# Kernel tuning notes

Measured on AMD Instinct MI355X. Metric: run time of the kernel, lower is better.

Reference implementation:

```python
import jax, jax.numpy as jnp
import numpy as np

ALPHA = 0.001      # module init arg alpha
BETA = 1.0         # softness of k-means assignments
N_ITERS = 10       # fixed soft-kmeans iterations
EPS = 1e-8


def _pairwise_sq_dist(x, c):
    # x: [N, D], c: [K, D] -> [N, K] squared euclidean distances
    x2 = jnp.sum(x * x, axis=1, keepdims=True)          # [N, 1]
    c2 = jnp.sum(c * c, axis=1)[None, :]                # [1, K]
    d2 = x2 + c2 - 2.0 * (x @ c.T)
    return jnp.maximum(d2, 0.0)


def soft_kmeans(enc, K):
    # deterministic init: first K points as centroids
    C = enc[:K]
    r = None
    loss = jnp.array(0.0, dtype=enc.dtype)
    for _ in range(N_ITERS):
        d2 = _pairwise_sq_dist(enc, C)                  # [N, K]
        r = jax.nn.softmax(-BETA * d2, axis=1)          # soft assignments [N, K]
        loss = jnp.mean(jnp.sum(r * d2, axis=1))        # weighted within-cluster dist
        C = (r.T @ enc) / (jnp.sum(r, axis=0)[:, None] + EPS)  # centroid update [K, D]
    return C, r, loss


def setup_inputs() -> dict:
    key = jax.random.key(0)
    k1, k2, k3 = jax.random.split(key, 3)
    N, D_DATA, D_LAT = 65536, 512, 64
    X = jax.random.normal(k1, (N, D_DATA), dtype=jnp.float32)
    encoding = jax.random.normal(k2, (N, D_LAT), dtype=jnp.float32)
    decoding = jax.random.normal(k3, (N, D_DATA), dtype=jnp.float32)
    return {"X": X, "encoding": encoding, "decoding": decoding, "K": 64}


def reference(X, encoding, decoding, K):
    decoder_loss = jnp.mean((X - decoding) ** 2)        # F.mse_loss (mean reduction)
    _, _, cluster_loss = soft_kmeans(encoding, K)
    return decoder_loss + cluster_loss * ALPHA
```

## Files before the change

kernel.cpp:

```cpp
#include <hip/hip_runtime.h>

typedef __attribute__((ext_vector_type(8))) short bf16x8;
typedef __attribute__((ext_vector_type(4))) float f32x4;

#define NROWS   65536
#define NSLICE  8
#define SLICESZ 4160
#define SETSZ   (NSLICE*SLICESZ)
#define EPSV    1e-8f
#define RPITCH  264

#define WS_DEC   0
#define WS_LOSS  1
#define WS_SETS  16
#define WS_X2    (WS_SETS + 9*SETSZ)
#define WS_ENCB  (WS_X2 + NROWS)
#define WS_EBF   (WS_ENCB + 2097152)
#define WS_END   (WS_EBF + 2097152)

static __device__ __forceinline__ unsigned short f2bf(float f) {
    union { float f; unsigned u; } v; v.f = f;
    unsigned u = v.u + 0x7fffu + ((v.u >> 16) & 1u);
    return (unsigned short)(u >> 16);
}
static __device__ __forceinline__ float bf2f(unsigned short h) {
    union { unsigned u; float f; } v; v.u = ((unsigned)h) << 16; return v.f;
}
static __device__ __forceinline__ uint4 pack8(const unsigned short* h) {
    uint4 o;
    o.x = h[0] | ((unsigned)h[1] << 16);
    o.y = h[2] | ((unsigned)h[3] << 16);
    o.z = h[4] | ((unsigned)h[5] << 16);
    o.w = h[6] | ((unsigned)h[7] << 16);
    return o;
}

__global__ __launch_bounds__(256, 4) void decoder_loss_kernel(
    const float* __restrict__ X, const float* __restrict__ Dec,
    float* __restrict__ out_sum)
{
    const int stride = 8192 * 256;
    int i = blockIdx.x * 256 + threadIdx.x;
    const f32x4* X4 = (const f32x4*)X;
    const f32x4* D4 = (const f32x4*)Dec;
    f32x4 va[4], vb[4];
    #pragma unroll
    for (int u = 0; u < 4; ++u) va[u] = __builtin_nontemporal_load(&X4[i + u * stride]);
    #pragma unroll
    for (int u = 0; u < 4; ++u) vb[u] = __builtin_nontemporal_load(&D4[i + u * stride]);
    float s0 = 0.f, s1 = 0.f, s2 = 0.f, s3 = 0.f;
    #pragma unroll
    for (int u = 0; u < 4; ++u) {
        f32x4 d = va[u] - vb[u];
        s0 = fmaf(d.x, d.x, s0);
        s1 = fmaf(d.y, d.y, s1);
        s2 = fmaf(d.z, d.z, s2);
        s3 = fmaf(d.w, d.w, s3);
    }
    float s = (s0 + s1) + (s2 + s3);
    #pragma unroll
    for (int off = 32; off; off >>= 1) s += __shfl_down(s, off, 64);
    __shared__ float red[4];
    if ((threadIdx.x & 63) == 0) red[threadIdx.x >> 6] = s;
    __syncthreads();
    if (threadIdx.x == 0) atomicAdd(out_sum, red[0] + red[1] + red[2] + red[3]);
}

__global__ __launch_bounds__(256) void prep0(
    const float* __restrict__ enc, unsigned* __restrict__ encB,
    uint4* __restrict__ encBfrag, float* __restrict__ x2)
{
    __shared__ unsigned short L[64 * 64];
    int t = threadIdx.x;
    int rl = t >> 2, part = t & 3;
    int row = blockIdx.x * 64 + rl;
    const float4* src = (const float4*)(enc + (size_t)row * 64 + part * 16);
    unsigned short hv[16];
    float ss = 0.f;
    #pragma unroll
    for (int i = 0; i < 4; ++i) {
        float4 v = src[i];
        unsigned short a = f2bf(v.x), b = f2bf(v.y), c = f2bf(v.z), d = f2bf(v.w);
        hv[i*4+0] = a; hv[i*4+1] = b; hv[i*4+2] = c; hv[i*4+3] = d;
        float fa = bf2f(a), fb = bf2f(b), fc = bf2f(c), fd = bf2f(d);
        ss = fmaf(fa, fa, fmaf(fb, fb, fmaf(fc, fc, fmaf(fd, fd, ss))));
    }
    unsigned* dst = encB + ((size_t)row * 64 + part * 16) / 2;
    #pragma unroll
    for (int i = 0; i < 8; ++i) dst[i] = (unsigned)hv[2*i] | ((unsigned)hv[2*i+1] << 16);
    #pragma unroll
    for (int i = 0; i < 16; ++i) L[rl * 64 + part * 16 + i] = hv[i];
    ss += __shfl_xor(ss, 1, 64);
    ss += __shfl_xor(ss, 2, 64);
    if (part == 0) x2[row] = ss;
    __syncthreads();
    for (int e = t; e < 512; e += 256) {
        int rbl = e >> 8, dt = (e >> 6) & 3, lane = e & 63;
        int q = lane >> 4, c = lane & 15;
        unsigned short hw[8];
        #pragma unroll
        for (int j = 0; j < 8; ++j)
            hw[j] = L[(rbl * 32 + q * 8 + j) * 64 + dt * 16 + c];
        encBfrag[(size_t)blockIdx.x * 512 + e] = pack8(hw);
    }
}

__global__ __launch_bounds__(256, 3) void kmeans_main(
    const bf16x8* __restrict__ encB8, const bf16x8* __restrict__ encBfrag8,
    const float* __restrict__ enc, const float* __restrict__ prev_set,
    float* __restrict__ cur_set, const float* __restrict__ x2,
    float* __restrict__ loss_sum, int mode)
{
    __shared__ union {
        unsigned short CsBf[4096];
        unsigned short rLT[64 * RPITCH];
    } U;
    __shared__ float x2L[256];
    __shared__ float c2L[64];
    __shared__ float rslL[64];
    __shared__ float rsumL[64];
    __shared__ float lredL[4];

    const int t = threadIdx.x;
    const int wave = t >> 6, lane = t & 63, q = lane >> 4, c = lane & 15;
    const int blockR0 = blockIdx.x * 256;

    x2L[t] = x2[blockR0 + t];
    if (t < 64) {
        rsumL[t] = 0.f;
        float v = 0.f;
        if (mode != 0) {
            #pragma unroll
            for (int sl = 0; sl < NSLICE; ++sl)
                v += prev_set[sl * SLICESZ + 4096 + t];
        }
        rslL[t] = 1.f / (v + EPSV);
    }
    __syncthreads();

    float c2part[4];
    #pragma unroll
    for (int j = 0; j < 4; ++j) {
        int v4 = t + j * 256;
        int row = v4 >> 4;
        float vx, vy, vz, vw;
        if (mode == 0) {
            f32x4 e = ((const f32x4*)enc)[v4];
            vx = e.x; vy = e.y; vz = e.z; vw = e.w;
        } else {
            float sx = 0.f, sy = 0.f, sz = 0.f, sw = 0.f;
            #pragma unroll
            for (int sl = 0; sl < NSLICE; ++sl) {
                f32x4 u = ((const f32x4*)(prev_set + (size_t)sl * SLICESZ))[v4];
                sx += u.x; sy += u.y; sz += u.z; sw += u.w;
            }
            float inv = rslL[row];
            vx = sx * inv; vy = sy * inv; vz = sz * inv; vw = sw * inv;
        }
        ushort4 h;
        h.x = f2bf(vx); h.y = f2bf(vy); h.z = f2bf(vz); h.w = f2bf(vw);
        ((ushort4*)U.CsBf)[v4] = h;
        float fx = bf2f(h.x), fy = bf2f(h.y), fz = bf2f(h.z), fw = bf2f(h.w);
        c2part[j] = fmaf(fx, fx, fmaf(fy, fy, fmaf(fz, fz, fw * fw)));
    }
    #pragma unroll
    for (int j = 0; j < 4; ++j) {
        float p = c2part[j];
        p += __shfl_xor(p, 1, 64); p += __shfl_xor(p, 2, 64);
        p += __shfl_xor(p, 4, 64); p += __shfl_xor(p, 8, 64);
        if ((lane & 15) == 0) c2L[j * 16 + (t >> 4)] = p;
    }
    __syncthreads();

    bf16x8 bfr[2][4];
    #pragma unroll
    for (int kk2 = 0; kk2 < 2; ++kk2)
        #pragma unroll
        for (int nt = 0; nt < 4; ++nt)
            bfr[kk2][nt] = *(const bf16x8*)&U.CsBf[(nt * 16 + c) * 64 + kk2 * 32 + q * 8];
    float c2f[4];
    #pragma unroll
    for (int nt = 0; nt < 4; ++nt) c2f[nt] = c2L[nt * 16 + c];
    __syncthreads();

    const f32x4 z4 = {0.f, 0.f, 0.f, 0.f};
    float rs[4] = {0.f, 0.f, 0.f, 0.f};
    float lossacc = 0.f;
    #pragma unroll
    for (int p = 0; p < 2; ++p) {
        bf16x8 a2f[4];
        #pragma unroll
        for (int sub = 0; sub < 2; ++sub) {
            int arow = blockR0 + p * 128 + wave * 32 + 8 * (c >> 2) + sub * 4 + (c & 3);
            const bf16x8* ap = encB8 + (size_t)arow * 8 + q;
            bf16x8 a0 = ap[0], a1 = ap[4];
            f32x4 accf[4];
            #pragma unroll
            for (int nt = 0; nt < 4; ++nt) {
                f32x4 s = __builtin_amdgcn_mfma_f32_16x16x32_bf16(a0, bfr[0][nt], z4, 0, 0, 0);
                accf[nt]  = __builtin_amdgcn_mfma_f32_16x16x32_bf16(a1, bfr[1][nt], s,  0, 0, 0);
            }
            #pragma unroll
            for (int reg = 0; reg < 4; ++reg) {
                int rloc = p * 128 + wave * 32 + 8 * q + sub * 4 + reg;
                float x2r = x2L[rloc];
                float d2[4], mn = 3.4e38f;
                #pragma unroll
                for (int nt = 0; nt < 4; ++nt) {
                    float v = fmaxf(x2r + c2f[nt] - 2.f * accf[nt][reg], 0.f);
                    d2[nt] = v; mn = fminf(mn, v);
                }
                mn = fminf(mn, __shfl_xor(mn, 1, 64));
                mn = fminf(mn, __shfl_xor(mn, 2, 64));
                mn = fminf(mn, __shfl_xor(mn, 4, 64));
                mn = fminf(mn, __shfl_xor(mn, 8, 64));
                float e[4], s = 0.f, swd = 0.f;
                #pragma unroll
                for (int nt = 0; nt < 4; ++nt) {
                    float ev = __expf(mn - d2[nt]);
                    e[nt] = ev; s += ev; swd = fmaf(ev, d2[nt], swd);
                }
                s   += __shfl_xor(s, 1, 64);   swd += __shfl_xor(swd, 1, 64);
                s   += __shfl_xor(s, 2, 64);   swd += __shfl_xor(swd, 2, 64);
                s   += __shfl_xor(s, 4, 64);   swd += __shfl_xor(swd, 4, 64);
                s   += __shfl_xor(s, 8, 64);   swd += __shfl_xor(swd, 8, 64);
                float inv = 1.f / s;
                if (mode == 2 && c == 0) lossacc += swd * inv;
                #pragma unroll
                for (int nt = 0; nt < 4; ++nt) {
                    float rv = e[nt] * inv;
                    rs[nt] += rv;
                    a2f[nt][sub * 4 + reg] = (short)f2bf(rv);
                }
            }
        }
        if (mode != 2) {
            #pragma unroll
            for (int nt = 0; nt < 4; ++nt)
                *(bf16x8*)&U.rLT[(nt * 16 + c) * RPITCH + p * 128 + wave * 32 + 8 * q] = a2f[nt];
        }
    }

    if (mode != 2) {
        #pragma unroll
        for (int nt = 0; nt < 4; ++nt) {
            float v = rs[nt];
            v += __shfl_xor(v, 16, 64);
            v += __shfl_xor(v, 32, 64);
            if (q == 0) atomicAdd(&rsumL[nt * 16 + c], v);
        }
        __syncthreads();

        const int mt = wave;
        f32x4 cacc[4];
        #pragma unroll
        for (int dt = 0; dt < 4; ++dt) cacc[dt] = z4;
        #pragma unroll
        for (int kk = 0; kk < 8; ++kk) {
            bf16x8 aA = *(const bf16x8*)&U.rLT[(mt * 16 + c) * RPITCH + kk * 32 + q * 8];
            #pragma unroll
            for (int dt = 0; dt < 4; ++dt) {
                bf16x8 bB = encBfrag8[((size_t)(blockIdx.x * 8 + kk) * 4 + dt) * 64 + lane];
                cacc[dt] = __builtin_amdgcn_mfma_f32_16x16x32_bf16(aA, bB, cacc[dt], 0, 0, 0);
            }
        }
        float* slice = cur_set + (size_t)(blockIdx.x & (NSLICE - 1)) * SLICESZ;
        #pragma unroll
        for (int dt = 0; dt < 4; ++dt)
            #pragma unroll
            for (int reg = 0; reg < 4; ++reg)
                atomicAdd(&slice[(mt * 16 + q * 4 + reg) * 64 + dt * 16 + c],
                          cacc[dt][reg]);
        if (t < 64) atomicAdd(&slice[4096 + t], rsumL[t]);
    } else {
        #pragma unroll
        for (int off = 32; off; off >>= 1) lossacc += __shfl_down(lossacc, off, 64);
        if (lane == 0) lredL[wave] = lossacc;
        __syncthreads();
        if (t == 0) atomicAdd(loss_sum, lredL[0] + lredL[1] + lredL[2] + lredL[3]);
    }
}

__global__ void finalize_kernel(const float* __restrict__ dec_sum,
                                const float* __restrict__ loss_sum,
                                float* __restrict__ out)
{
    out[0] = dec_sum[0] * (1.f / (65536.f * 512.f))
           + 0.001f * (loss_sum[0] * (1.f / 65536.f));
}

extern "C" void kernel_launch(void* const* d_in, const int* in_sizes, int n_in,
                              void* d_out, int out_size, void* d_ws, size_t ws_size,
                              hipStream_t stream)
{
    const float* X   = (const float*)d_in[0];
    const float* enc = (const float*)d_in[1];
    const float* dec = (const float*)d_in[2];

    float* ws = (float*)d_ws;
    float* dec_sum  = ws + WS_DEC;
    float* loss_sum = ws + WS_LOSS;
    float* sets = ws + WS_SETS;
    float* x2   = ws + WS_X2;
    unsigned* encB  = (unsigned*)(ws + WS_ENCB);
    uint4* encBfrag = (uint4*)(ws + WS_EBF);

    hipMemsetAsync(d_ws, 0, (size_t)WS_X2 * sizeof(float), stream);

    decoder_loss_kernel<<<dim3(8192), dim3(256), 0, stream>>>(X, dec, dec_sum);
    prep0<<<dim3(1024), dim3(256), 0, stream>>>(enc, encB, encBfrag, x2);

    const bf16x8* encB8 = (const bf16x8*)encB;
    const bf16x8* eBf8  = (const bf16x8*)encBfrag;

    for (int it = 0; it < 10; ++it) {
        int mode = (it == 0) ? 0 : ((it == 9) ? 2 : 1);
        const float* prev = (it == 0) ? sets : sets + (size_t)(it - 1) * SETSZ;
        float* cur = (it < 9) ? sets + (size_t)it * SETSZ : sets;
        kmeans_main<<<dim3(256), dim3(256), 0, stream>>>(
            encB8, eBf8, enc, prev, cur, x2, loss_sum, mode);
    }
    finalize_kernel<<<1, 1, 0, stream>>>(dec_sum, loss_sum, (float*)d_out);
}
```

Baseline: 489.2 us.

## Fold decoder MSE reduction into kmeans iteration launches as extra blocks

Removes the standalone decoder-loss kernel and splits its streaming MSE over X and decoding into 8 chunks. Each of the first 8 kmeans iteration launches gets 256 extra blocks that each reduce one chunk. The kmeans grid uses only 256 blocks and leaves CUs idle, so the bandwidth-bound reduction can overlap with the latency-bound kmeans work. The costs are more atomics on dec_sum and possible contention for memory bandwidth or CU slots with the kmeans blocks.

```diff
diff --git a/kernel.cpp b/kernel.cpp
--- a/kernel.cpp
+++ b/kernel.cpp
@@ -9,6 +9,10 @@
 #define SETSZ   (NSLICE*SLICESZ)
 #define EPSV    1e-8f
 #define RPITCH  264
+
+#define KB      256
+#define SB      256
+#define SCHUNK  1048576
 
 #define WS_DEC   0
 #define WS_LOSS  1
@@ -33,37 +37,6 @@
     o.z = h[4] | ((unsigned)h[5] << 16);
     o.w = h[6] | ((unsigned)h[7] << 16);
     return o;
-}
-
-__global__ __launch_bounds__(256, 4) void decoder_loss_kernel(
-    const float* __restrict__ X, const float* __restrict__ Dec,
-    float* __restrict__ out_sum)
-{
-    const int stride = 8192 * 256;
-    int i = blockIdx.x * 256 + threadIdx.x;
-    const f32x4* X4 = (const f32x4*)X;
-    const f32x4* D4 = (const f32x4*)Dec;
-    f32x4 va[4], vb[4];
-    #pragma unroll
-    for (int u = 0; u < 4; ++u) va[u] = __builtin_nontemporal_load(&X4[i + u * stride]);
-    #pragma unroll
-    for (int u = 0; u < 4; ++u) vb[u] = __builtin_nontemporal_load(&D4[i + u * stride]);
-    float s0 = 0.f, s1 = 0.f, s2 = 0.f, s3 = 0.f;
-    #pragma unroll
-    for (int u = 0; u < 4; ++u) {
-        f32x4 d = va[u] - vb[u];
-        s0 = fmaf(d.x, d.x, s0);
-        s1 = fmaf(d.y, d.y, s1);
-        s2 = fmaf(d.z, d.z, s2);
-        s3 = fmaf(d.w, d.w, s3);
-    }
-    float s = (s0 + s1) + (s2 + s3);
-    #pragma unroll
-    for (int off = 32; off; off >>= 1) s += __shfl_down(s, off, 64);
-    __shared__ float red[4];
-    if ((threadIdx.x & 63) == 0) red[threadIdx.x >> 6] = s;
-    __syncthreads();
-    if (threadIdx.x == 0) atomicAdd(out_sum, red[0] + red[1] + red[2] + red[3]);
 }
 
 __global__ __launch_bounds__(256) void prep0(
@@ -109,8 +82,39 @@
     const bf16x8* __restrict__ encB8, const bf16x8* __restrict__ encBfrag8,
     const float* __restrict__ enc, const float* __restrict__ prev_set,
     float* __restrict__ cur_set, const float* __restrict__ x2,
-    float* __restrict__ loss_sum, int mode)
+    float* __restrict__ loss_sum, int mode,
+    const f32x4* __restrict__ Xs, const f32x4* __restrict__ Ds,
+    float* __restrict__ dec_sum, int itchunk)
 {
+    if (blockIdx.x >= KB) {
+        const int tid = (blockIdx.x - KB) * 256 + threadIdx.x;
+        const size_t base = (size_t)itchunk * SCHUNK + tid;
+        float s0 = 0.f, s1 = 0.f, s2 = 0.f, s3 = 0.f;
+        #pragma unroll
+        for (int h = 0; h < 2; ++h) {
+            f32x4 xv[8], dv[8];
+            #pragma unroll
+            for (int u = 0; u < 8; ++u)
+                xv[u] = __builtin_nontemporal_load(&Xs[base + (size_t)(h * 8 + u) * 65536]);
+            #pragma unroll
+            for (int u = 0; u < 8; ++u)
+                dv[u] = __builtin_nontemporal_load(&Ds[base + (size_t)(h * 8 + u) * 65536]);
+            #pragma unroll
+            for (int u = 0; u < 8; ++u) {
+                f32x4 d = xv[u] - dv[u];
+                s0 = fmaf(d.x, d.x, s0);
+                s1 = fmaf(d.y, d.y, s1);
+                s2 = fmaf(d.z, d.z, s2);
+                s3 = fmaf(d.w, d.w, s3);
+            }
+        }
+        float s = (s0 + s1) + (s2 + s3);
+        #pragma unroll
+        for (int off = 32; off; off >>= 1) s += __shfl_down(s, off, 64);
+        if ((threadIdx.x & 63) == 0) atomicAdd(dec_sum, s);
+        return;
+    }
+
     __shared__ union {
         unsigned short CsBf[4096];
         unsigned short rLT[64 * RPITCH];
@@ -307,7 +311,6 @@
 
     hipMemsetAsync(d_ws, 0, (size_t)WS_X2 * sizeof(float), stream);
 
-    decoder_loss_kernel<<<dim3(8192), dim3(256), 0, stream>>>(X, dec, dec_sum);
     prep0<<<dim3(1024), dim3(256), 0, stream>>>(enc, encB, encBfrag, x2);
 
     const bf16x8* encB8 = (const bf16x8*)encB;
@@ -317,8 +320,10 @@
         int mode = (it == 0) ? 0 : ((it == 9) ? 2 : 1);
         const float* prev = (it == 0) ? sets : sets + (size_t)(it - 1) * SETSZ;
         float* cur = (it < 9) ? sets + (size_t)it * SETSZ : sets;
-        kmeans_main<<<dim3(256), dim3(256), 0, stream>>>(
-            encB8, eBf8, enc, prev, cur, x2, loss_sum, mode);
+        int grid = (it < 8) ? (KB + SB) : KB;
+        kmeans_main<<<dim3(grid), dim3(256), 0, stream>>>(
+            encB8, eBf8, enc, prev, cur, x2, loss_sum, mode,
+            (const f32x4*)X, (const f32x4*)dec, dec_sum, it);
     }
     finalize_kernel<<<1, 1, 0, stream>>>(dec_sum, loss_sum, (float*)d_out);
 }
```

New measurement: 478.7 us. 2.1% less time.

## Halve rows per k-means block to double the grid and restructure decoder loss

Applied to the files above, without the earlier changes.

The k-means kernel now handles 128 rows per block instead of 256 and launches 512 blocks, so more CUs get work on each of the ten iterations. Its launch bound drops to 2 blocks per CU, and the centroid-update MFMA loop shrinks to match the smaller row tile. The decoder MSE kernel now uses fewer blocks that each do 16 plain vector loads per thread instead of 4 nontemporal ones, and it runs after the k-means loop rather than before it. In exchange, the centroid slices receive twice as many atomic adds, and each block carries proportionally more fixed setup cost.

```diff
diff --git a/kernel.cpp b/kernel.cpp
--- a/kernel.cpp
+++ b/kernel.cpp
@@ -9,6 +9,9 @@
 #define SETSZ   (NSLICE*SLICESZ)
 #define EPSV    1e-8f
 #define RPITCH  264
+
+#define KB      512
+#define RPB     128
 
 #define WS_DEC   0
 #define WS_LOSS  1
@@ -36,26 +39,24 @@
 }
 
 __global__ __launch_bounds__(256, 4) void decoder_loss_kernel(
-    const float* __restrict__ X, const float* __restrict__ Dec,
+    const f32x4* __restrict__ X4, const f32x4* __restrict__ D4,
     float* __restrict__ out_sum)
 {
-    const int stride = 8192 * 256;
-    int i = blockIdx.x * 256 + threadIdx.x;
-    const f32x4* X4 = (const f32x4*)X;
-    const f32x4* D4 = (const f32x4*)Dec;
-    f32x4 va[4], vb[4];
-    #pragma unroll
-    for (int u = 0; u < 4; ++u) va[u] = __builtin_nontemporal_load(&X4[i + u * stride]);
-    #pragma unroll
-    for (int u = 0; u < 4; ++u) vb[u] = __builtin_nontemporal_load(&D4[i + u * stride]);
+    const size_t tid = (size_t)blockIdx.x * 256 + threadIdx.x;
     float s0 = 0.f, s1 = 0.f, s2 = 0.f, s3 = 0.f;
     #pragma unroll
-    for (int u = 0; u < 4; ++u) {
-        f32x4 d = va[u] - vb[u];
-        s0 = fmaf(d.x, d.x, s0);
-        s1 = fmaf(d.y, d.y, s1);
-        s2 = fmaf(d.z, d.z, s2);
-        s3 = fmaf(d.w, d.w, s3);
+    for (int i = 0; i < 4; ++i) {
+        f32x4 xv[4], dv[4];
+        #pragma unroll
+        for (int j = 0; j < 4; ++j) xv[j] = X4[tid + (size_t)(i * 4 + j) * 524288];
+        #pragma unroll
+        for (int j = 0; j < 4; ++j) dv[j] = D4[tid + (size_t)(i * 4 + j) * 524288];
+        #pragma unroll
+        for (int j = 0; j < 4; ++j) {
+            f32x4 d = xv[j] - dv[j];
+            s0 = fmaf(d.x, d.x, s0); s1 = fmaf(d.y, d.y, s1);
+            s2 = fmaf(d.z, d.z, s2); s3 = fmaf(d.w, d.w, s3);
+        }
     }
     float s = (s0 + s1) + (s2 + s3);
     #pragma unroll
@@ -105,7 +106,7 @@
     }
 }
 
-__global__ __launch_bounds__(256, 3) void kmeans_main(
+__global__ __launch_bounds__(256, 2) void kmeans_main(
     const bf16x8* __restrict__ encB8, const bf16x8* __restrict__ encBfrag8,
     const float* __restrict__ enc, const float* __restrict__ prev_set,
     float* __restrict__ cur_set, const float* __restrict__ x2,
@@ -115,7 +116,7 @@
         unsigned short CsBf[4096];
         unsigned short rLT[64 * RPITCH];
     } U;
-    __shared__ float x2L[256];
+    __shared__ float x2L[RPB];
     __shared__ float c2L[64];
     __shared__ float rslL[64];
     __shared__ float rsumL[64];
@@ -123,9 +124,9 @@
 
     const int t = threadIdx.x;
     const int wave = t >> 6, lane = t & 63, q = lane >> 4, c = lane & 15;
-    const int blockR0 = blockIdx.x * 256;
-
-    x2L[t] = x2[blockR0 + t];
+    const int blockR0 = blockIdx.x * RPB;
+
+    if (t < RPB) x2L[t] = x2[blockR0 + t];
     if (t < 64) {
         rsumL[t] = 0.f;
         float v = 0.f;
@@ -186,12 +187,11 @@
     const f32x4 z4 = {0.f, 0.f, 0.f, 0.f};
     float rs[4] = {0.f, 0.f, 0.f, 0.f};
     float lossacc = 0.f;
-    #pragma unroll
-    for (int p = 0; p < 2; ++p) {
+    {
         bf16x8 a2f[4];
         #pragma unroll
         for (int sub = 0; sub < 2; ++sub) {
-            int arow = blockR0 + p * 128 + wave * 32 + 8 * (c >> 2) + sub * 4 + (c & 3);
+            int arow = blockR0 + wave * 32 + 8 * (c >> 2) + sub * 4 + (c & 3);
             const bf16x8* ap = encB8 + (size_t)arow * 8 + q;
             bf16x8 a0 = ap[0], a1 = ap[4];
             f32x4 accf[4];
@@ -202,7 +202,7 @@
             }
             #pragma unroll
             for (int reg = 0; reg < 4; ++reg) {
-                int rloc = p * 128 + wave * 32 + 8 * q + sub * 4 + reg;
+                int rloc = wave * 32 + 8 * q + sub * 4 + reg;
                 float x2r = x2L[rloc];
                 float d2[4], mn = 3.4e38f;
                 #pragma unroll
@@ -237,7 +237,7 @@
         if (mode != 2) {
             #pragma unroll
             for (int nt = 0; nt < 4; ++nt)
-                *(bf16x8*)&U.rLT[(nt * 16 + c) * RPITCH + p * 128 + wave * 32 + 8 * q] = a2f[nt];
+                *(bf16x8*)&U.rLT[(nt * 16 + c) * RPITCH + wave * 32 + 8 * q] = a2f[nt];
         }
     }
 
@@ -256,11 +256,11 @@
         #pragma unroll
         for (int dt = 0; dt < 4; ++dt) cacc[dt] = z4;
         #pragma unroll
-        for (int kk = 0; kk < 8; ++kk) {
+        for (int kk = 0; kk < 4; ++kk) {
             bf16x8 aA = *(const bf16x8*)&U.rLT[(mt * 16 + c) * RPITCH + kk * 32 + q * 8];
             #pragma unroll
             for (int dt = 0; dt < 4; ++dt) {
-                bf16x8 bB = encBfrag8[((size_t)(blockIdx.x * 8 + kk) * 4 + dt) * 64 + lane];
+                bf16x8 bB = encBfrag8[((size_t)(blockIdx.x * 4 + kk) * 4 + dt) * 64 + lane];
                 cacc[dt] = __builtin_amdgcn_mfma_f32_16x16x32_bf16(aA, bB, cacc[dt], 0, 0, 0);
             }
         }
@@ -307,7 +307,6 @@
 
     hipMemsetAsync(d_ws, 0, (size_t)WS_X2 * sizeof(float), stream);
 
-    decoder_loss_kernel<<<dim3(8192), dim3(256), 0, stream>>>(X, dec, dec_sum);
     prep0<<<dim3(1024), dim3(256), 0, stream>>>(enc, encB, encBfrag, x2);
 
     const bf16x8* encB8 = (const bf16x8*)encB;
@@ -317,8 +316,12 @@
         int mode = (it == 0) ? 0 : ((it == 9) ? 2 : 1);
         const float* prev = (it == 0) ? sets : sets + (size_t)(it - 1) * SETSZ;
         float* cur = (it < 9) ? sets + (size_t)it * SETSZ : sets;
-        kmeans_main<<<dim3(256), dim3(256), 0, stream>>>(
+        kmeans_main<<<dim3(KB), dim3(256), 0, stream>>>(
             encB8, eBf8, enc, prev, cur, x2, loss_sum, mode);
     }
+
+    decoder_loss_kernel<<<dim3(2048), dim3(256), 0, stream>>>(
+        (const f32x4*)X, (const f32x4*)dec, dec_sum);
+
     finalize_kernel<<<1, 1, 0, stream>>>(dec_sum, loss_sum, (float*)d_out);
 }
```

After: 462.7 us. 1.06x faster.
